# Optimization experiments

Hardware: AMD Instinct MI355X
Metric: run time of the kernel (lower is better)

Reference implementation:

```python
import jax, jax.numpy as jnp
import numpy as np

B, IN_UNITS, N_CAPS = 64, 64, 2048
NUM_UNITS, UNIT_SIZE = 32, 16


def setup_inputs() -> dict:
    key = jax.random.key(0)
    k1, k2, k3, k4 = jax.random.split(key, 4)
    x = jax.random.normal(k1, (B, IN_UNITS, N_CAPS), dtype=jnp.float32)
    # kaiming-uniform-ish init for W1; W2/b2 are zero-init in the original but we
    # randomize (small) so the reference math is non-degenerate.
    bound = float(np.sqrt(6.0 / IN_UNITS))
    W1 = jax.random.uniform(k2, (NUM_UNITS, UNIT_SIZE, IN_UNITS), dtype=jnp.float32,
                            minval=-bound, maxval=bound)
    W2 = 0.05 * jax.random.normal(k3, (UNIT_SIZE, IN_UNITS), dtype=jnp.float32)
    b2 = 0.05 * jax.random.normal(k4, (UNIT_SIZE,), dtype=jnp.float32)
    return {"x": x, "W1": W1, "W2": W2, "b2": b2}


def reference(x, W1, W2, b2):
    # x: (B, in_units, N) -> (B, N, in_units)
    xT = jnp.transpose(x, (0, 2, 1))
    # u_hat: (B, N, num_units, unit_size)  (original keeps a trailing singleton dim)
    u_hat = jnp.einsum('bni,kui->bnku', xT, W1)
    # logit: identical across num_units (W2 is stacked/broadcast in the original)
    logit = jnp.einsum('bni,ui->bnu', xT, W2)[:, :, None, :] + b2  # (B, N, 1, U)
    logit = jnp.broadcast_to(logit, u_hat.shape)                   # (B, N, K, U)
    cij = jax.nn.softmax(logit, axis=2)  # softmax over num_units
    # activation: L2 norm of input pose over in_units -> (B, N, 1, 1)
    a = jnp.linalg.norm(xT, axis=2)[:, :, None, None]
    ar = a * cij                                   # (B, N, K, U)
    coeff = ar / ar.sum(axis=1, keepdims=True)     # normalize over input capsules
    pose_out = (coeff * u_hat).sum(axis=1)         # (B, K, U)
    return pose_out
```

## Files before the change

kernel.cpp:

```cpp
#include <hip/hip_runtime.h>
#include <math.h>


#define BB 64
#define IN_UNITS 64
#define NCAPS 2048
#define OUT_PER_B 512
#define CHUNKS 16
#define TILE_N 128

__global__ __launch_bounds__(256) void sr_pass1(
    const float* __restrict__ x, float* __restrict__ z_part, float* __restrict__ s_part)
{
  __shared__ __align__(16) float xt[IN_UNITS][TILE_N];
  __shared__ float4 ssqp[8][32];
  __shared__ __align__(16) float a_lds[TILE_N];
  __shared__ float ztmp[4][IN_UNITS];
  __shared__ float swave[2];

  const int bid   = blockIdx.x;
  const int b     = bid >> 4;
  const int chunk = bid & 15;
  const int n0    = chunk * TILE_N;
  const int t     = threadIdx.x;

  const int q  = t & 31;
  const int ih = t >> 5;

  const float* xb = x + (size_t)b * IN_UNITS * NCAPS + n0;
  float4 ssq4 = make_float4(0.f, 0.f, 0.f, 0.f);
  #pragma unroll
  for (int j = 0; j < 8; ++j) {
    const int r = ih * 8 + j;
    float4 xv = reinterpret_cast<const float4*>(xb + (size_t)r * NCAPS)[q];
    ssq4.x = fmaf(xv.x, xv.x, ssq4.x);
    ssq4.y = fmaf(xv.y, xv.y, ssq4.y);
    ssq4.z = fmaf(xv.z, xv.z, ssq4.z);
    ssq4.w = fmaf(xv.w, xv.w, ssq4.w);
    reinterpret_cast<float4*>(&xt[r][0])[q ^ (r & 7)] = xv;
  }
  ssqp[ih][q] = ssq4;
  __syncthreads();

  float a = 0.f;
  if (t < TILE_N) {
    const int nq = t >> 2, c = t & 3;
    float ss = 0.f;
    #pragma unroll
    for (int k = 0; k < 8; ++k)
      ss += reinterpret_cast<const float*>(&ssqp[k][nq])[c];
    a = sqrtf(ss);
    a_lds[t] = a;
  }
  float s = a;
  #pragma unroll
  for (int off = 32; off > 0; off >>= 1) s += __shfl_down(s, off, 64);
  if ((t & 63) == 0 && t < 128) swave[t >> 6] = s;
  __syncthreads();
  if (t == 0) s_part[b * CHUNKS + chunk] = swave[0] + swave[1];

  const int i  = t & 63;
  const int tg = t >> 6;
  const float4* a4 = reinterpret_cast<const float4*>(a_lds);
  float acc = 0.f;
  #pragma unroll
  for (int m = 0; m < 8; ++m) {
    const int qq = tg * 8 + m;
    float4 xv = reinterpret_cast<const float4*>(&xt[i][0])[qq ^ (i & 7)];
    float4 av = a4[qq];
    acc = fmaf(xv.x, av.x, acc);
    acc = fmaf(xv.y, av.y, acc);
    acc = fmaf(xv.z, av.z, acc);
    acc = fmaf(xv.w, av.w, acc);
  }
  ztmp[tg][i] = acc;
  __syncthreads();
  if (t < IN_UNITS) {
    z_part[((size_t)b * CHUNKS + chunk) * IN_UNITS + t] =
        ztmp[0][t] + ztmp[1][t] + ztmp[2][t] + ztmp[3][t];
  }
}

__global__ __launch_bounds__(256) void sr_pass2(
    const float* __restrict__ z_part, const float* __restrict__ s_part,
    const float* __restrict__ W1, float* __restrict__ out)
{
  __shared__ __align__(16) float z_lds[IN_UNITS];
  const int bid = blockIdx.x;
  const int b   = bid >> 3;
  const int g   = bid & 7;
  const int t   = threadIdx.x;

  if (t < IN_UNITS) {
    float zz = 0.f;
    #pragma unroll
    for (int c = 0; c < CHUNKS; ++c)
      zz += z_part[((size_t)b * CHUNKS + c) * IN_UNITS + t];
    z_lds[t] = zz;
  }
  float ss = 0.f;
  #pragma unroll
  for (int c = 0; c < CHUNKS; ++c) ss += s_part[b * CHUNKS + c];
  const float sinv = 1.0f / ss;
  __syncthreads();

  const int jl   = t >> 2;
  const int part = t & 3;
  const int j    = g * 64 + jl;
  const float4* w4 = reinterpret_cast<const float4*>(W1 + (size_t)j * IN_UNITS + part * 16);
  const float4* z4 = reinterpret_cast<const float4*>(z_lds) + part * 4;
  float acc = 0.f;
  #pragma unroll
  for (int jj = 0; jj < 4; ++jj) {
    float4 wv = w4[jj];
    float4 zv = z4[jj];
    acc = fmaf(wv.x, zv.x, acc);
    acc = fmaf(wv.y, zv.y, acc);
    acc = fmaf(wv.z, zv.z, acc);
    acc = fmaf(wv.w, zv.w, acc);
  }
  acc += __shfl_xor(acc, 1);
  acc += __shfl_xor(acc, 2);
  if (part == 0) out[(size_t)b * OUT_PER_B + j] = acc * sinv;
}

extern "C" void kernel_launch(void* const* d_in, const int* in_sizes, int n_in,
                              void* d_out, int out_size, void* d_ws, size_t ws_size,
                              hipStream_t stream) {
  const float* x  = (const float*)d_in[0];
  const float* W1 = (const float*)d_in[1];
  float* out = (float*)d_out;

  float* z_part = (float*)d_ws;
  float* s_part = z_part + (size_t)BB * CHUNKS * IN_UNITS;

  sr_pass1<<<dim3(BB * CHUNKS), dim3(256), 0, stream>>>(x, z_part, s_part);
  sr_pass2<<<dim3(BB * 8), dim3(256), 0, stream>>>(z_part, s_part, W1, out);
}
```

Baseline: 13.59 us.

## Keep x tile in registers and reduce via wave shuffles instead of LDS transpose

Pass 1 no longer stages the x tile in shared memory. Each thread keeps its eight float4 loads in registers and computes the sum of squares and the a-weighted row dot products directly, reducing across lanes with shuffles, which removes the LDS transpose, one barrier and the ztmp stage. Pass 2 now spreads the chunk reduction of z_part over all 256 threads with an LDS combine step, adding one extra barrier. The cost is more shuffle instructions and higher register pressure per thread.

```diff
diff --git a/kernel.cpp b/kernel.cpp
--- a/kernel.cpp
+++ b/kernel.cpp
@@ -12,10 +12,8 @@
 __global__ __launch_bounds__(256) void sr_pass1(
     const float* __restrict__ x, float* __restrict__ z_part, float* __restrict__ s_part)
 {
-  __shared__ __align__(16) float xt[IN_UNITS][TILE_N];
-  __shared__ float4 ssqp[8][32];
+  __shared__ float4 ssqp[4][32];
   __shared__ __align__(16) float a_lds[TILE_N];
-  __shared__ float ztmp[4][IN_UNITS];
   __shared__ float swave[2];
 
   const int bid   = blockIdx.x;
@@ -24,60 +22,89 @@
   const int n0    = chunk * TILE_N;
   const int t     = threadIdx.x;
 
-  const int q  = t & 31;
-  const int ih = t >> 5;
+  const int q = t & 31;
+  const int g = t >> 5;
 
   const float* xb = x + (size_t)b * IN_UNITS * NCAPS + n0;
-  float4 ssq4 = make_float4(0.f, 0.f, 0.f, 0.f);
-  #pragma unroll
-  for (int j = 0; j < 8; ++j) {
-    const int r = ih * 8 + j;
-    float4 xv = reinterpret_cast<const float4*>(xb + (size_t)r * NCAPS)[q];
-    ssq4.x = fmaf(xv.x, xv.x, ssq4.x);
-    ssq4.y = fmaf(xv.y, xv.y, ssq4.y);
-    ssq4.z = fmaf(xv.z, xv.z, ssq4.z);
-    ssq4.w = fmaf(xv.w, xv.w, ssq4.w);
-    reinterpret_cast<float4*>(&xt[r][0])[q ^ (r & 7)] = xv;
+  float4 xv0, xv1, xv2, xv3, xv4, xv5, xv6, xv7;
+  {
+    const size_t r0 = (size_t)(g * 8) * NCAPS;
+    xv0 = reinterpret_cast<const float4*>(xb + r0)[q];
+    xv1 = reinterpret_cast<const float4*>(xb + r0 + NCAPS)[q];
+    xv2 = reinterpret_cast<const float4*>(xb + r0 + 2 * NCAPS)[q];
+    xv3 = reinterpret_cast<const float4*>(xb + r0 + 3 * NCAPS)[q];
+    xv4 = reinterpret_cast<const float4*>(xb + r0 + 4 * NCAPS)[q];
+    xv5 = reinterpret_cast<const float4*>(xb + r0 + 5 * NCAPS)[q];
+    xv6 = reinterpret_cast<const float4*>(xb + r0 + 6 * NCAPS)[q];
+    xv7 = reinterpret_cast<const float4*>(xb + r0 + 7 * NCAPS)[q];
   }
-  ssqp[ih][q] = ssq4;
+  float4 ssq4;
+  ssq4.x = xv0.x * xv0.x; ssq4.y = xv0.y * xv0.y;
+  ssq4.z = xv0.z * xv0.z; ssq4.w = xv0.w * xv0.w;
+  ssq4.x = fmaf(xv1.x, xv1.x, ssq4.x); ssq4.y = fmaf(xv1.y, xv1.y, ssq4.y);
+  ssq4.z = fmaf(xv1.z, xv1.z, ssq4.z); ssq4.w = fmaf(xv1.w, xv1.w, ssq4.w);
+  ssq4.x = fmaf(xv2.x, xv2.x, ssq4.x); ssq4.y = fmaf(xv2.y, xv2.y, ssq4.y);
+  ssq4.z = fmaf(xv2.z, xv2.z, ssq4.z); ssq4.w = fmaf(xv2.w, xv2.w, ssq4.w);
+  ssq4.x = fmaf(xv3.x, xv3.x, ssq4.x); ssq4.y = fmaf(xv3.y, xv3.y, ssq4.y);
+  ssq4.z = fmaf(xv3.z, xv3.z, ssq4.z); ssq4.w = fmaf(xv3.w, xv3.w, ssq4.w);
+  ssq4.x = fmaf(xv4.x, xv4.x, ssq4.x); ssq4.y = fmaf(xv4.y, xv4.y, ssq4.y);
+  ssq4.z = fmaf(xv4.z, xv4.z, ssq4.z); ssq4.w = fmaf(xv4.w, xv4.w, ssq4.w);
+  ssq4.x = fmaf(xv5.x, xv5.x, ssq4.x); ssq4.y = fmaf(xv5.y, xv5.y, ssq4.y);
+  ssq4.z = fmaf(xv5.z, xv5.z, ssq4.z); ssq4.w = fmaf(xv5.w, xv5.w, ssq4.w);
+  ssq4.x = fmaf(xv6.x, xv6.x, ssq4.x); ssq4.y = fmaf(xv6.y, xv6.y, ssq4.y);
+  ssq4.z = fmaf(xv6.z, xv6.z, ssq4.z); ssq4.w = fmaf(xv6.w, xv6.w, ssq4.w);
+  ssq4.x = fmaf(xv7.x, xv7.x, ssq4.x); ssq4.y = fmaf(xv7.y, xv7.y, ssq4.y);
+  ssq4.z = fmaf(xv7.z, xv7.z, ssq4.z); ssq4.w = fmaf(xv7.w, xv7.w, ssq4.w);
+
+  ssq4.x += __shfl_xor(ssq4.x, 32, 64);
+  ssq4.y += __shfl_xor(ssq4.y, 32, 64);
+  ssq4.z += __shfl_xor(ssq4.z, 32, 64);
+  ssq4.w += __shfl_xor(ssq4.w, 32, 64);
+  if ((g & 1) == 0) ssqp[g >> 1][q] = ssq4;
   __syncthreads();
 
-  float a = 0.f;
   if (t < TILE_N) {
     const int nq = t >> 2, c = t & 3;
     float ss = 0.f;
     #pragma unroll
-    for (int k = 0; k < 8; ++k)
+    for (int k = 0; k < 4; ++k)
       ss += reinterpret_cast<const float*>(&ssqp[k][nq])[c];
-    a = sqrtf(ss);
+    float a = sqrtf(ss);
     a_lds[t] = a;
+    float s = a;
+    #pragma unroll
+    for (int off = 32; off > 0; off >>= 1) s += __shfl_down(s, off, 64);
+    if ((t & 63) == 0) swave[t >> 6] = s;
   }
-  float s = a;
-  #pragma unroll
-  for (int off = 32; off > 0; off >>= 1) s += __shfl_down(s, off, 64);
-  if ((t & 63) == 0 && t < 128) swave[t >> 6] = s;
   __syncthreads();
   if (t == 0) s_part[b * CHUNKS + chunk] = swave[0] + swave[1];
 
-  const int i  = t & 63;
-  const int tg = t >> 6;
-  const float4* a4 = reinterpret_cast<const float4*>(a_lds);
-  float acc = 0.f;
+  const float4 av = reinterpret_cast<const float4*>(a_lds)[q];
+  float z0, z1, z2, z3, z4, z5, z6, z7;
+  z0 = fmaf(xv0.x, av.x, fmaf(xv0.y, av.y, fmaf(xv0.z, av.z, xv0.w * av.w)));
+  z1 = fmaf(xv1.x, av.x, fmaf(xv1.y, av.y, fmaf(xv1.z, av.z, xv1.w * av.w)));
+  z2 = fmaf(xv2.x, av.x, fmaf(xv2.y, av.y, fmaf(xv2.z, av.z, xv2.w * av.w)));
+  z3 = fmaf(xv3.x, av.x, fmaf(xv3.y, av.y, fmaf(xv3.z, av.z, xv3.w * av.w)));
+  z4 = fmaf(xv4.x, av.x, fmaf(xv4.y, av.y, fmaf(xv4.z, av.z, xv4.w * av.w)));
+  z5 = fmaf(xv5.x, av.x, fmaf(xv5.y, av.y, fmaf(xv5.z, av.z, xv5.w * av.w)));
+  z6 = fmaf(xv6.x, av.x, fmaf(xv6.y, av.y, fmaf(xv6.z, av.z, xv6.w * av.w)));
+  z7 = fmaf(xv7.x, av.x, fmaf(xv7.y, av.y, fmaf(xv7.z, av.z, xv7.w * av.w)));
+
   #pragma unroll
-  for (int m = 0; m < 8; ++m) {
-    const int qq = tg * 8 + m;
-    float4 xv = reinterpret_cast<const float4*>(&xt[i][0])[qq ^ (i & 7)];
-    float4 av = a4[qq];
-    acc = fmaf(xv.x, av.x, acc);
-    acc = fmaf(xv.y, av.y, acc);
-    acc = fmaf(xv.z, av.z, acc);
-    acc = fmaf(xv.w, av.w, acc);
+  for (int m = 1; m < 32; m <<= 1) {
+    z0 += __shfl_xor(z0, m, 64);
+    z1 += __shfl_xor(z1, m, 64);
+    z2 += __shfl_xor(z2, m, 64);
+    z3 += __shfl_xor(z3, m, 64);
+    z4 += __shfl_xor(z4, m, 64);
+    z5 += __shfl_xor(z5, m, 64);
+    z6 += __shfl_xor(z6, m, 64);
+    z7 += __shfl_xor(z7, m, 64);
   }
-  ztmp[tg][i] = acc;
-  __syncthreads();
-  if (t < IN_UNITS) {
-    z_part[((size_t)b * CHUNKS + chunk) * IN_UNITS + t] =
-        ztmp[0][t] + ztmp[1][t] + ztmp[2][t] + ztmp[3][t];
+  if (q == 0) {
+    float* zp = z_part + ((size_t)b * CHUNKS + chunk) * IN_UNITS + g * 8;
+    reinterpret_cast<float4*>(zp)[0] = make_float4(z0, z1, z2, z3);
+    reinterpret_cast<float4*>(zp)[1] = make_float4(z4, z5, z6, z7);
   }
 }
 
@@ -85,30 +112,34 @@
     const float* __restrict__ z_part, const float* __restrict__ s_part,
     const float* __restrict__ W1, float* __restrict__ out)
 {
-  __shared__ __align__(16) float z_lds[IN_UNITS];
+  __shared__ float ztmp[4][IN_UNITS];
+  __shared__ __align__(16) float z_l[IN_UNITS];
   const int bid = blockIdx.x;
   const int b   = bid >> 3;
   const int g   = bid & 7;
   const int t   = threadIdx.x;
 
-  if (t < IN_UNITS) {
+  {
+    const int i = t & 63, tg = t >> 6;
     float zz = 0.f;
     #pragma unroll
-    for (int c = 0; c < CHUNKS; ++c)
-      zz += z_part[((size_t)b * CHUNKS + c) * IN_UNITS + t];
-    z_lds[t] = zz;
+    for (int k = 0; k < 4; ++k)
+      zz += z_part[((size_t)b * CHUNKS + tg * 4 + k) * IN_UNITS + i];
+    ztmp[tg][i] = zz;
   }
   float ss = 0.f;
   #pragma unroll
   for (int c = 0; c < CHUNKS; ++c) ss += s_part[b * CHUNKS + c];
   const float sinv = 1.0f / ss;
   __syncthreads();
+  if (t < IN_UNITS) z_l[t] = ztmp[0][t] + ztmp[1][t] + ztmp[2][t] + ztmp[3][t];
+  __syncthreads();
 
   const int jl   = t >> 2;
   const int part = t & 3;
   const int j    = g * 64 + jl;
   const float4* w4 = reinterpret_cast<const float4*>(W1 + (size_t)j * IN_UNITS + part * 16);
-  const float4* z4 = reinterpret_cast<const float4*>(z_lds) + part * 4;
+  const float4* z4 = reinterpret_cast<const float4*>(z_l) + part * 4;
   float acc = 0.f;
   #pragma unroll
   for (int jj = 0; jj < 4; ++jj) {
```

After: 14.24 us. +4.8%, slower.
